# Kernel tuning notes

Measured on AMD Instinct MI355X. Metric: run time of the kernel, lower is better.

Reference implementation:

```python
import jax, jax.numpy as jnp
import numpy as np

EPS = 1e-6

def feature_map(x):
    # 'elu' feature map: elu(x) + 1 (positive feature map from Katharopoulos et al.)
    return jax.nn.elu(x) + 1.0

def setup_inputs() -> dict:
    key = jax.random.key(0)
    kq, kk, kv = jax.random.split(key, 3)
    B, L, H, D = 4, 2048, 16, 64
    q = jax.random.normal(kq, (B, L, H, D), dtype=jnp.float32)
    k = jax.random.normal(kk, (B, L, H, D), dtype=jnp.float32)
    v = jax.random.normal(kv, (B, L, H, D), dtype=jnp.float32)
    return {"q": q, "k": k, "v": v}

def reference(q, k, v):
    # q, k, v: [N, L, H, D]  (attention_mask=None -> causal linear attention)
    qf = feature_map(q)
    kf = feature_map(k)
    # normalizer: z[n,l,h] = sum_d qf[n,l,h,d] * cumsum_s<=l kf[n,s,h,d]
    z = jnp.einsum('nlhd,nlhd->nlh', qf, jnp.cumsum(kf, axis=1)) + EPS
    # causal_dot_product via scan over sequence with carry S[n,h,d,m]
    B, L, H, D = q.shape
    M = v.shape[-1]
    qs = jnp.moveaxis(qf, 1, 0)  # [L, N, H, D]
    ks = jnp.moveaxis(kf, 1, 0)
    vs = jnp.moveaxis(v, 1, 0)

    def step(S, qkv):
        ql, kl, vl = qkv                              # [N,H,D], [N,H,D], [N,H,M]
        S = S + jnp.einsum('nhd,nhm->nhdm', kl, vl)   # running sum of k v^T
        out = jnp.einsum('nhd,nhdm->nhm', ql, S)
        return S, out

    S0 = jnp.zeros((B, H, D, M), dtype=q.dtype)
    _, outs = jax.lax.scan(step, S0, (qs, ks, vs))    # outs: [L, N, H, M]
    v_ = jnp.moveaxis(outs, 0, 1)                     # [N, L, H, M]
    return v_ / z[..., None]
```

## Files before the change

### kernel.cpp

```cpp
#include <hip/hip_runtime.h>
#include <cstdint>

#define LL 2048
#define HH 16
#define DD 64
#define LSTR 1024
#define EPSF 1e-6f
#define PAD 72
#define SWZ(row, off) ((row)*PAD + ((off) ^ ((((row)>>3)&7)<<3)))

typedef __bf16 bf16x8 __attribute__((ext_vector_type(8)));
typedef float floatx4 __attribute__((ext_vector_type(4)));
typedef unsigned short ushortx8 __attribute__((ext_vector_type(8)));
typedef unsigned short ushortx4 __attribute__((ext_vector_type(4)));
typedef unsigned short ushortx2 __attribute__((ext_vector_type(2)));

static __device__ __forceinline__ float fmap(float x){ return x > 0.f ? x + 1.f : __expf(x); }
static __device__ __forceinline__ unsigned short f2bf(float f){
    return __builtin_bit_cast(unsigned short, static_cast<__bf16>(f));
}
static __device__ __forceinline__ float bf2f(unsigned short s){
    unsigned u = ((unsigned)s) << 16;
    return __builtin_bit_cast(float, u);
}
static __device__ __forceinline__ bf16x8 ldf(const unsigned short* p){
    return __builtin_bit_cast(bf16x8, *(const ushortx8*)p);
}

template<bool MAP>
static __device__ __forceinline__ void st_sd(unsigned short* base, int r, int c, float4 a, float4 b){
    if (MAP) {
        *(ushortx4*)(base + r*PAD + c)     = ushortx4{ f2bf(fmap(a.x)), f2bf(fmap(a.y)), f2bf(fmap(a.z)), f2bf(fmap(a.w)) };
        *(ushortx4*)(base + (r+1)*PAD + c) = ushortx4{ f2bf(fmap(b.x)), f2bf(fmap(b.y)), f2bf(fmap(b.z)), f2bf(fmap(b.w)) };
    } else {
        *(ushortx4*)(base + r*PAD + c)     = ushortx4{ f2bf(a.x), f2bf(a.y), f2bf(a.z), f2bf(a.w) };
        *(ushortx4*)(base + (r+1)*PAD + c) = ushortx4{ f2bf(b.x), f2bf(b.y), f2bf(b.z), f2bf(b.w) };
    }
}
template<bool MAP>
static __device__ __forceinline__ void st_tr(unsigned short* base, int r, int c, float4 a, float4 b){
    float aa[4] = {a.x, a.y, a.z, a.w}, bb[4] = {b.x, b.y, b.z, b.w};
#pragma unroll
    for (int e = 0; e < 4; ++e) {
        float x0 = MAP ? fmap(aa[e]) : aa[e];
        float x1 = MAP ? fmap(bb[e]) : bb[e];
        *(ushortx2*)(base + SWZ(c+e, r)) = ushortx2{ f2bf(x0), f2bf(x1) };
    }
}

__global__ __launch_bounds__(512) void kA(const float* __restrict__ kp, const float* __restrict__ vp,
                                          unsigned short* __restrict__ snap, float* __restrict__ ksnap)
{
    __shared__ __align__(16) unsigned short kft[2][DD*PAD];
    __shared__ __align__(16) unsigned short vtt[2][DD*PAD];
    const int blk = blockIdx.x;
    const int bh = blk >> 3, oct = blk & 7, b = bh >> 4, h = bh & 15;
    const int t = threadIdx.x;
    const int w = t >> 6, lane = t & 63, quad = lane >> 4, lr = lane & 15;
    const int m0 = 16*(w & 3), dth = (w >> 2) << 1;
    const int l0s = (t >> 4) * 2, col4 = (t & 15) << 2;

    floatx4 acc[2];
    acc[0] = floatx4{0.f,0.f,0.f,0.f};
    acc[1] = floatx4{0.f,0.f,0.f,0.f};
    float ksa = 0.f;

    const int64_t gb0 = ((int64_t)(b*LL + oct*256)*HH + h)*DD;
    {
        const float* gk = kp + gb0 + (int64_t)l0s*LSTR + col4;
        const float* gv = vp + gb0 + (int64_t)l0s*LSTR + col4;
        float4 ka = *(const float4*)gk, kb = *(const float4*)(gk + LSTR);
        float4 va = *(const float4*)gv, vb = *(const float4*)(gv + LSTR);
        st_tr<true >(kft[0], l0s, col4, ka, kb);
        st_tr<false>(vtt[0], l0s, col4, va, vb);
    }
    __syncthreads();

#pragma unroll 1
    for (int sc = 0; sc < 4; ++sc) {
        const int p = sc & 1;
        float4 ka, kb, va, vb;
        if (sc < 3) {
            const int64_t gb = gb0 + (int64_t)(sc+1)*DD*LSTR;
            const float* gk = kp + gb + (int64_t)l0s*LSTR + col4;
            const float* gv = vp + gb + (int64_t)l0s*LSTR + col4;
            ka = *(const float4*)gk; kb = *(const float4*)(gk + LSTR);
            va = *(const float4*)gv; vb = *(const float4*)(gv + LSTR);
        }
#pragma unroll
        for (int kk = 0; kk < 2; ++kk) {
            bf16x8 a = ldf(vtt[p] + SWZ(m0+lr, kk*32 + quad*8));
#pragma unroll
            for (int dtl = 0; dtl < 2; ++dtl) {
                bf16x8 bbf = ldf(kft[p] + SWZ((dth+dtl)*16+lr, kk*32 + quad*8));
                acc[dtl] = __builtin_amdgcn_mfma_f32_16x16x32_bf16(a, bbf, acc[dtl], 0, 0, 0);
            }
        }
        {
            unsigned short* so = snap + ((int64_t)blk*4 + sc)*4096;
#pragma unroll
            for (int dtl = 0; dtl < 2; ++dtl)
#pragma unroll
                for (int r = 0; r < 4; ++r)
                    so[(m0 + quad*4 + r)*DD + (dth+dtl)*16 + lr] = f2bf(acc[dtl][r]);
        }
        if (t < DD) {
#pragma unroll
            for (int jj = 0; jj < 8; ++jj) {
                ushortx8 u = *(const ushortx8*)(kft[p] + SWZ(t, jj*8));
#pragma unroll
                for (int e = 0; e < 8; ++e) ksa += bf2f(u[e]);
            }
            ksnap[((int64_t)blk*4 + sc)*DD + t] = ksa;
        }
        if (sc < 3) {
            st_tr<true >(kft[p^1], l0s, col4, ka, kb);
            st_tr<false>(vtt[p^1], l0s, col4, va, vb);
        }
        __syncthreads();
    }
}

__global__ __launch_bounds__(256, 4) void kC(const float* __restrict__ qp, const float* __restrict__ kp,
                                             const float* __restrict__ vp,
                                             const unsigned short* __restrict__ snap,
                                             const float* __restrict__ ksnap,
                                             float* __restrict__ outp)
{
    __shared__ __align__(16) unsigned short kfx[DD*PAD];
    __shared__ __align__(16) unsigned short vtt[DD*PAD];
    __shared__ __align__(16) unsigned short sld[DD*PAD];
    const int bid = blockIdx.x;
    const int bh = bid >> 5, c = bid & 31, b = bh >> 4, h = bh & 15;
    const int o = c >> 2, j = c & 3;
    const int t = threadIdx.x;
    const int w = t >> 6, lane = t & 63, quad = lane >> 4, lr = lane & 15;
    const int l0 = 16*w;
    const int64_t gbase = ((int64_t)(b*LL + c*DD)*HH + h)*DD;
    const int64_t so8 = (int64_t)bh*8;

    float qv[16];
    {
        const float* gq = qp + gbase + (int64_t)(l0+lr)*LSTR;
        float4 a0 = *(const float4*)(gq + quad*8);
        float4 a1 = *(const float4*)(gq + quad*8 + 4);
        float4 a2 = *(const float4*)(gq + 32 + quad*8);
        float4 a3 = *(const float4*)(gq + 32 + quad*8 + 4);
        qv[0]=fmap(a0.x); qv[1]=fmap(a0.y); qv[2]=fmap(a0.z); qv[3]=fmap(a0.w);
        qv[4]=fmap(a1.x); qv[5]=fmap(a1.y); qv[6]=fmap(a1.z); qv[7]=fmap(a1.w);
        qv[8]=fmap(a2.x); qv[9]=fmap(a2.y); qv[10]=fmap(a2.z); qv[11]=fmap(a2.w);
        qv[12]=fmap(a3.x); qv[13]=fmap(a3.y); qv[14]=fmap(a3.z); qv[15]=fmap(a3.w);
    }

    {
        const int sm = t >> 2, sd0 = (t & 3) << 4;
        float sa[16];
#pragma unroll
        for (int e = 0; e < 16; ++e) sa[e] = 0.f;
#pragma unroll
        for (int op = 0; op < 7; ++op)
            if (op < o) {
                const unsigned short* sp = snap + ((so8 + op)*4 + 3)*4096 + sm*DD + sd0;
                ushortx8 u0 = *(const ushortx8*)sp, u1 = *(const ushortx8*)(sp + 8);
#pragma unroll
                for (int e = 0; e < 8; ++e) { sa[e] += bf2f(u0[e]); sa[8+e] += bf2f(u1[e]); }
            }
        if (j > 0) {
            const unsigned short* sp = snap + ((so8 + o)*4 + (j-1))*4096 + sm*DD + sd0;
            ushortx8 u0 = *(const ushortx8*)sp, u1 = *(const ushortx8*)(sp + 8);
#pragma unroll
            for (int e = 0; e < 8; ++e) { sa[e] += bf2f(u0[e]); sa[8+e] += bf2f(u1[e]); }
        }
        ushortx8 w0, w1;
#pragma unroll
        for (int e = 0; e < 8; ++e) { w0[e] = f2bf(sa[e]); w1[e] = f2bf(sa[8+e]); }
        *(ushortx8*)(sld + sm*PAD + sd0)     = w0;
        *(ushortx8*)(sld + sm*PAD + sd0 + 8) = w1;
    }

    float zfull = 0.f;
    {
        float kp16[16];
#pragma unroll
        for (int e = 0; e < 16; ++e) kp16[e] = 0.f;
#pragma unroll
        for (int op = 0; op < 7; ++op)
            if (op < o) {
                const float* kb = ksnap + ((so8 + op)*4 + 3)*DD;
                float4 x0 = *(const float4*)(kb + quad*8);
                float4 x1 = *(const float4*)(kb + quad*8 + 4);
                float4 x2 = *(const float4*)(kb + 32 + quad*8);
                float4 x3 = *(const float4*)(kb + 32 + quad*8 + 4);
                kp16[0]+=x0.x; kp16[1]+=x0.y; kp16[2]+=x0.z; kp16[3]+=x0.w;
                kp16[4]+=x1.x; kp16[5]+=x1.y; kp16[6]+=x1.z; kp16[7]+=x1.w;
                kp16[8]+=x2.x; kp16[9]+=x2.y; kp16[10]+=x2.z; kp16[11]+=x2.w;
                kp16[12]+=x3.x; kp16[13]+=x3.y; kp16[14]+=x3.z; kp16[15]+=x3.w;
            }
        if (j > 0) {
            const float* kb = ksnap + ((so8 + o)*4 + (j-1))*DD;
            float4 x0 = *(const float4*)(kb + quad*8);
            float4 x1 = *(const float4*)(kb + quad*8 + 4);
            float4 x2 = *(const float4*)(kb + 32 + quad*8);
            float4 x3 = *(const float4*)(kb + 32 + quad*8 + 4);
            kp16[0]+=x0.x; kp16[1]+=x0.y; kp16[2]+=x0.z; kp16[3]+=x0.w;
            kp16[4]+=x1.x; kp16[5]+=x1.y; kp16[6]+=x1.z; kp16[7]+=x1.w;
            kp16[8]+=x2.x; kp16[9]+=x2.y; kp16[10]+=x2.z; kp16[11]+=x2.w;
            kp16[12]+=x3.x; kp16[13]+=x3.y; kp16[14]+=x3.z; kp16[15]+=x3.w;
        }
#pragma unroll
        for (int e = 0; e < 16; ++e) zfull += qv[e] * kp16[e];
        zfull += __shfl_xor(zfull, 16, 64);
        zfull += __shfl_xor(zfull, 32, 64);
    }

    bf16x8 aq0, aq1;
#pragma unroll
    for (int e = 0; e < 8; ++e) { aq0[e] = (__bf16)qv[e]; aq1[e] = (__bf16)qv[8+e]; }

#pragma unroll
    for (int i = 0; i < 2; ++i) {
        int flat = t + 256*i;
        int l0s = (flat >> 4) * 2, col = (flat & 15) << 2;
        const float* gk = kp + gbase + (int64_t)l0s*LSTR + col;
        const float* gv = vp + gbase + (int64_t)l0s*LSTR + col;
        float4 ka = *(const float4*)(gk), kb = *(const float4*)(gk + LSTR);
        float4 va = *(const float4*)(gv), vb = *(const float4*)(gv + LSTR);
        st_sd<true >(kfx, l0s, col, ka, kb);
        st_tr<false>(vtt, l0s, col, va, vb);
    }
    __syncthreads();

    floatx4 sc4[4];
#pragma unroll
    for (int tt = 0; tt < 4; ++tt) sc4[tt] = floatx4{0.f,0.f,0.f,0.f};
#pragma unroll
    for (int kk = 0; kk < 2; ++kk) {
        bf16x8 aqk = kk ? aq1 : aq0;
#pragma unroll
        for (int tt = 0; tt < 4; ++tt) {
            bf16x8 bb = ldf(kfx + (tt*16+lr)*PAD + kk*32 + quad*8);
            sc4[tt] = __builtin_amdgcn_mfma_f32_16x16x32_bf16(aqk, bb, sc4[tt], 0, 0, 0);
        }
    }
    __syncthreads();

    float zp[4] = {0.f,0.f,0.f,0.f};
#pragma unroll
    for (int tt = 0; tt < 4; ++tt)
#pragma unroll
        for (int r = 0; r < 4; ++r) {
            int row = l0 + quad*4 + r;
            int col = tt*16 + lr;
            float val = (col <= row) ? sc4[tt][r] : 0.f;
            zp[r] += val;
            kfx[row*PAD + col] = f2bf(val);
        }
#pragma unroll
    for (int m = 1; m < 16; m <<= 1)
#pragma unroll
        for (int r = 0; r < 4; ++r) zp[r] += __shfl_xor(zp[r], m, 64);
    float rz[4];
#pragma unroll
    for (int r = 0; r < 4; ++r) {
        zp[r] += __shfl(zfull, quad*20 + r, 64);
        rz[r] = 1.f / (zp[r] + EPSF);
    }

    floatx4 oa[4];
#pragma unroll
    for (int mt = 0; mt < 4; ++mt) oa[mt] = floatx4{0.f,0.f,0.f,0.f};
#pragma unroll
    for (int kk = 0; kk < 2; ++kk) {
        bf16x8 a2 = ldf(kfx + (l0+lr)*PAD + kk*32 + quad*8);
#pragma unroll
        for (int mt = 0; mt < 4; ++mt) {
            bf16x8 bv = ldf(vtt + SWZ(mt*16+lr, kk*32 + quad*8));
            oa[mt] = __builtin_amdgcn_mfma_f32_16x16x32_bf16(a2, bv, oa[mt], 0, 0, 0);
        }
    }
#pragma unroll
    for (int kk = 0; kk < 2; ++kk) {
        bf16x8 aqk = kk ? aq1 : aq0;
#pragma unroll
        for (int mt = 0; mt < 4; ++mt) {
            bf16x8 bs = ldf(sld + (mt*16+lr)*PAD + kk*32 + quad*8);
            oa[mt] = __builtin_amdgcn_mfma_f32_16x16x32_bf16(aqk, bs, oa[mt], 0, 0, 0);
        }
    }
#pragma unroll
    for (int r = 0; r < 4; ++r) {
        int row = l0 + quad*4 + r;
#pragma unroll
        for (int mt = 0; mt < 4; ++mt)
            outp[gbase + (int64_t)row*LSTR + mt*16 + lr] = oa[mt][r] * rz[r];
    }
}

extern "C" void kernel_launch(void* const* d_in, const int* in_sizes, int n_in,
                              void* d_out, int out_size, void* d_ws, size_t ws_size,
                              hipStream_t stream) {
    const float* q = (const float*)d_in[0];
    const float* k = (const float*)d_in[1];
    const float* v = (const float*)d_in[2];
    float* out = (float*)d_out;
    char* ws = (char*)d_ws;
    unsigned short* snap = (unsigned short*)ws;
    float* ksnap = (float*)(ws + (size_t)512*4*4096*2);
    kA<<<512,  512, 0, stream>>>(k, v, snap, ksnap);
    kC<<<2048, 256, 0, stream>>>(q, k, v, snap, ksnap, out);
}
```

Measured before the change: 157.5 us.

## Merge four chunk blocks into one looping block with double-buffered prefetch

```diff
diff --git a/kernel.cpp b/kernel.cpp
--- a/kernel.cpp
+++ b/kernel.cpp
@@ -53,8 +53,9 @@
 {
     __shared__ __align__(16) unsigned short kft[2][DD*PAD];
     __shared__ __align__(16) unsigned short vtt[2][DD*PAD];
-    const int blk = blockIdx.x;
-    const int bh = blk >> 3, oct = blk & 7, b = bh >> 4, h = bh & 15;
+    const int orig = blockIdx.x;
+    const int oct = orig >> 6, bh = orig & 63, b = bh >> 4, h = bh & 15;
+    const int64_t sblk = (int64_t)bh*8 + oct;
     const int t = threadIdx.x;
     const int w = t >> 6, lane = t & 63, quad = lane >> 4, lr = lane & 15;
     const int m0 = 16*(w & 3), dth = (w >> 2) << 1;
@@ -97,7 +98,7 @@
             }
         }
         {
-            unsigned short* so = snap + ((int64_t)blk*4 + sc)*4096;
+            unsigned short* so = snap + (sblk*4 + sc)*4096;
 #pragma unroll
             for (int dtl = 0; dtl < 2; ++dtl)
 #pragma unroll
@@ -111,7 +112,7 @@
 #pragma unroll
                 for (int e = 0; e < 8; ++e) ksa += bf2f(u[e]);
             }
-            ksnap[((int64_t)blk*4 + sc)*DD + t] = ksa;
+            ksnap[(sblk*4 + sc)*DD + t] = ksa;
         }
         if (sc < 3) {
             st_tr<true >(kft[p^1], l0s, col4, ka, kb);
@@ -121,178 +122,178 @@
     }
 }
 
-__global__ __launch_bounds__(256, 4) void kC(const float* __restrict__ qp, const float* __restrict__ kp,
+__global__ __launch_bounds__(512, 2) void kD(const float* __restrict__ qp, const float* __restrict__ kp,
                                              const float* __restrict__ vp,
                                              const unsigned short* __restrict__ snap,
                                              const float* __restrict__ ksnap,
                                              float* __restrict__ outp)
 {
-    __shared__ __align__(16) unsigned short kfx[DD*PAD];
-    __shared__ __align__(16) unsigned short vtt[DD*PAD];
+    __shared__ __align__(16) unsigned short qls[2][DD*PAD];
+    __shared__ __align__(16) unsigned short kfx[2][DD*PAD];
+    __shared__ __align__(16) unsigned short vtt[2][DD*PAD];
+    __shared__ __align__(16) unsigned short sct[DD*PAD];
     __shared__ __align__(16) unsigned short sld[DD*PAD];
-    const int bid = blockIdx.x;
-    const int bh = bid >> 5, c = bid & 31, b = bh >> 4, h = bh & 15;
-    const int o = c >> 2, j = c & 3;
+    __shared__ float zp2[2][DD];
+    __shared__ float kzb[DD];
+    __shared__ float kzs[2][DD];
+
+    const int orig = blockIdx.x;
+    const int o = orig >> 6, bh = orig & 63, b = bh >> 4, h = bh & 15;
     const int t = threadIdx.x;
     const int w = t >> 6, lane = t & 63, quad = lane >> 4, lr = lane & 15;
-    const int l0 = 16*w;
-    const int64_t gbase = ((int64_t)(b*LL + c*DD)*HH + h)*DD;
-    const int64_t so8 = (int64_t)bh*8;
-
-    float qv[16];
+    const int wi = w >> 1, wj = w & 1;
+    const int l0 = 16*wi;
+    const int l0s = (t >> 4) * 2, col4 = (t & 15) << 2;
+    const int sm = t >> 3, sd0 = (t & 7) << 3;
+    const int64_t bhb = ((int64_t)b*LL*HH + h)*DD;
+    const int64_t sb8 = (int64_t)bh*8;
+
+    float sbase[8];
+#pragma unroll
+    for (int e = 0; e < 8; ++e) sbase[e] = 0.f;
+#pragma unroll
+    for (int op = 0; op < 7; ++op)
+        if (op < o) {
+            ushortx8 u = *(const ushortx8*)(snap + ((sb8+op)*4 + 3)*4096 + sm*DD + sd0);
+#pragma unroll
+            for (int e = 0; e < 8; ++e) sbase[e] += bf2f(u[e]);
+        }
     {
-        const float* gq = qp + gbase + (int64_t)(l0+lr)*LSTR;
-        float4 a0 = *(const float4*)(gq + quad*8);
-        float4 a1 = *(const float4*)(gq + quad*8 + 4);
-        float4 a2 = *(const float4*)(gq + 32 + quad*8);
-        float4 a3 = *(const float4*)(gq + 32 + quad*8 + 4);
-        qv[0]=fmap(a0.x); qv[1]=fmap(a0.y); qv[2]=fmap(a0.z); qv[3]=fmap(a0.w);
-        qv[4]=fmap(a1.x); qv[5]=fmap(a1.y); qv[6]=fmap(a1.z); qv[7]=fmap(a1.w);
-        qv[8]=fmap(a2.x); qv[9]=fmap(a2.y); qv[10]=fmap(a2.z); qv[11]=fmap(a2.w);
-        qv[12]=fmap(a3.x); qv[13]=fmap(a3.y); qv[14]=fmap(a3.z); qv[15]=fmap(a3.w);
-    }
-
-    {
-        const int sm = t >> 2, sd0 = (t & 3) << 4;
-        float sa[16];
-#pragma unroll
-        for (int e = 0; e < 16; ++e) sa[e] = 0.f;
+        ushortx8 w0;
+#pragma unroll
+        for (int e = 0; e < 8; ++e) w0[e] = f2bf(sbase[e]);
+        *(ushortx8*)(sld + sm*PAD + sd0) = w0;
+    }
+    if (t < 16) {
+        float a0=0.f, a1=0.f, a2=0.f, a3=0.f;
 #pragma unroll
         for (int op = 0; op < 7; ++op)
             if (op < o) {
-                const unsigned short* sp = snap + ((so8 + op)*4 + 3)*4096 + sm*DD + sd0;
-                ushortx8 u0 = *(const ushortx8*)sp, u1 = *(const ushortx8*)(sp + 8);
-#pragma unroll
-                for (int e = 0; e < 8; ++e) { sa[e] += bf2f(u0[e]); sa[8+e] += bf2f(u1[e]); }
-            }
+                float4 x = *(const float4*)(ksnap + ((sb8+op)*4 + 3)*DD + t*4);
+                a0 += x.x; a1 += x.y; a2 += x.z; a3 += x.w;
+            }
+        *(float4*)(kzb + t*4) = float4{a0,a1,a2,a3};
+    }
+    {
+        const int64_t gb = bhb + (int64_t)(o*4)*DD*LSTR;
+        const float* gq = qp + gb + (int64_t)l0s*LSTR + col4;
+        const float* gk = kp + gb + (int64_t)l0s*LSTR + col4;
+        const float* gv = vp + gb + (int64_t)l0s*LSTR + col4;
+        float4 q0 = *(const float4*)gq, q1 = *(const float4*)(gq + LSTR);
+        float4 k0 = *(const float4*)gk, k1 = *(const float4*)(gk + LSTR);
+        float4 v0 = *(const float4*)gv, v1 = *(const float4*)(gv + LSTR);
+        st_sd<true >(qls[0], l0s, col4, q0, q1);
+        st_sd<true >(kfx[0], l0s, col4, k0, k1);
+        st_tr<false>(vtt[0], l0s, col4, v0, v1);
+    }
+    __syncthreads();
+
+    ushortx8 usn = ushortx8{0,0,0,0,0,0,0,0};
+    float4 cq0, cq1, ck0, ck1, cv0, cv1;
+
+#pragma unroll 1
+    for (int j = 0; j < 4; ++j) {
+        const int p = j & 1;
+        const int64_t gb = bhb + (int64_t)(o*4 + j)*DD*LSTR;
         if (j > 0) {
-            const unsigned short* sp = snap + ((so8 + o)*4 + (j-1))*4096 + sm*DD + sd0;
-            ushortx8 u0 = *(const ushortx8*)sp, u1 = *(const ushortx8*)(sp + 8);
-#pragma unroll
-            for (int e = 0; e < 8; ++e) { sa[e] += bf2f(u0[e]); sa[8+e] += bf2f(u1[e]); }
-        }
-        ushortx8 w0, w1;
-#pragma unroll
-        for (int e = 0; e < 8; ++e) { w0[e] = f2bf(sa[e]); w1[e] = f2bf(sa[8+e]); }
-        *(ushortx8*)(sld + sm*PAD + sd0)     = w0;
-        *(ushortx8*)(sld + sm*PAD + sd0 + 8) = w1;
-    }
-
-    float zfull = 0.f;
-    {
-        float kp16[16];
-#pragma unroll
-        for (int e = 0; e < 16; ++e) kp16[e] = 0.f;
-#pragma unroll
-        for (int op = 0; op < 7; ++op)
-            if (op < o) {
-                const float* kb = ksnap + ((so8 + op)*4 + 3)*DD;
-                float4 x0 = *(const float4*)(kb + quad*8);
-                float4 x1 = *(const float4*)(kb + quad*8 + 4);
-                float4 x2 = *(const float4*)(kb + 32 + quad*8);
-                float4 x3 = *(const float4*)(kb + 32 + quad*8 + 4);
-                kp16[0]+=x0.x; kp16[1]+=x0.y; kp16[2]+=x0.z; kp16[3]+=x0.w;
-                kp16[4]+=x1.x; kp16[5]+=x1.y; kp16[6]+=x1.z; kp16[7]+=x1.w;
-                kp16[8]+=x2.x; kp16[9]+=x2.y; kp16[10]+=x2.z; kp16[11]+=x2.w;
-                kp16[12]+=x3.x; kp16[13]+=x3.y; kp16[14]+=x3.z; kp16[15]+=x3.w;
-            }
-        if (j > 0) {
-            const float* kb = ksnap + ((so8 + o)*4 + (j-1))*DD;
-            float4 x0 = *(const float4*)(kb + quad*8);
-            float4 x1 = *(const float4*)(kb + quad*8 + 4);
-            float4 x2 = *(const float4*)(kb + 32 + quad*8);
-            float4 x3 = *(const float4*)(kb + 32 + quad*8 + 4);
-            kp16[0]+=x0.x; kp16[1]+=x0.y; kp16[2]+=x0.z; kp16[3]+=x0.w;
-            kp16[4]+=x1.x; kp16[5]+=x1.y; kp16[6]+=x1.z; kp16[7]+=x1.w;
-            kp16[8]+=x2.x; kp16[9]+=x2.y; kp16[10]+=x2.z; kp16[11]+=x2.w;
-            kp16[12]+=x3.x; kp16[13]+=x3.y; kp16[14]+=x3.z; kp16[15]+=x3.w;
-        }
-#pragma unroll
-        for (int e = 0; e < 16; ++e) zfull += qv[e] * kp16[e];
-        zfull += __shfl_xor(zfull, 16, 64);
-        zfull += __shfl_xor(zfull, 32, 64);
-    }
-
-    bf16x8 aq0, aq1;
-#pragma unroll
-    for (int e = 0; e < 8; ++e) { aq0[e] = (__bf16)qv[e]; aq1[e] = (__bf16)qv[8+e]; }
-
-#pragma unroll
-    for (int i = 0; i < 2; ++i) {
-        int flat = t + 256*i;
-        int l0s = (flat >> 4) * 2, col = (flat & 15) << 2;
-        const float* gk = kp + gbase + (int64_t)l0s*LSTR + col;
-        const float* gv = vp + gbase + (int64_t)l0s*LSTR + col;
-        float4 ka = *(const float4*)(gk), kb = *(const float4*)(gk + LSTR);
-        float4 va = *(const float4*)(gv), vb = *(const float4*)(gv + LSTR);
-        st_sd<true >(kfx, l0s, col, ka, kb);
-        st_tr<false>(vtt, l0s, col, va, vb);
-    }
-    __syncthreads();
-
-    floatx4 sc4[4];
-#pragma unroll
-    for (int tt = 0; tt < 4; ++tt) sc4[tt] = floatx4{0.f,0.f,0.f,0.f};
-#pragma unroll
-    for (int kk = 0; kk < 2; ++kk) {
-        bf16x8 aqk = kk ? aq1 : aq0;
-#pragma unroll
-        for (int tt = 0; tt < 4; ++tt) {
-            bf16x8 bb = ldf(kfx + (tt*16+lr)*PAD + kk*32 + quad*8);
-            sc4[tt] = __builtin_amdgcn_mfma_f32_16x16x32_bf16(aqk, bb, sc4[tt], 0, 0, 0);
-        }
-    }
-    __syncthreads();
-
-    float zp[4] = {0.f,0.f,0.f,0.f};
-#pragma unroll
-    for (int tt = 0; tt < 4; ++tt)
+            ushortx8 w0;
+#pragma unroll
+            for (int e = 0; e < 8; ++e) w0[e] = f2bf(sbase[e] + bf2f(usn[e]));
+            *(ushortx8*)(sld + sm*PAD + sd0) = w0;
+        }
+        bf16x8 aq0 = ldf(qls[p] + (l0+lr)*PAD + quad*8);
+        bf16x8 aq1 = ldf(qls[p] + (l0+lr)*PAD + 32 + quad*8);
+        float zfull = 0.f;
+        {
+            const float* kc = (j == 0) ? kzb : kzs[j & 1];
+#pragma unroll
+            for (int e = 0; e < 8; ++e) zfull += (float)aq0[e] * kc[quad*8 + e];
+#pragma unroll
+            for (int e = 0; e < 8; ++e) zfull += (float)aq1[e] * kc[32 + quad*8 + e];
+            zfull += __shfl_xor(zfull, 16, 64);
+            zfull += __shfl_xor(zfull, 32, 64);
+        }
+        if (j < 3) {
+            const int64_t gn = bhb + (int64_t)(o*4 + j + 1)*DD*LSTR;
+            const float* gq = qp + gn + (int64_t)l0s*LSTR + col4;
+            const float* gk = kp + gn + (int64_t)l0s*LSTR + col4;
+            const float* gv = vp + gn + (int64_t)l0s*LSTR + col4;
+            cq0 = *(const float4*)gq; cq1 = *(const float4*)(gq + LSTR);
+            ck0 = *(const float4*)gk; ck1 = *(const float4*)(gk + LSTR);
+            cv0 = *(const float4*)gv; cv1 = *(const float4*)(gv + LSTR);
+            usn = *(const ushortx8*)(snap + ((sb8+o)*4 + j)*4096 + sm*DD + sd0);
+            if (t < 16) {
+                float4 x = *(const float4*)(ksnap + ((sb8+o)*4 + j)*DD + t*4);
+                float4 zb = *(const float4*)(kzb + t*4);
+                *(float4*)(kzs[(j+1)&1] + t*4) = float4{zb.x+x.x, zb.y+x.y, zb.z+x.z, zb.w+x.w};
+            }
+        }
+        floatx4 s0 = floatx4{0.f,0.f,0.f,0.f}, s1 = floatx4{0.f,0.f,0.f,0.f};
+#pragma unroll
+        for (int kk = 0; kk < 2; ++kk) {
+            bf16x8 aqk = kk ? aq1 : aq0;
+            bf16x8 b0 = ldf(kfx[p] + ((2*wj+0)*16+lr)*PAD + kk*32 + quad*8);
+            bf16x8 b1 = ldf(kfx[p] + ((2*wj+1)*16+lr)*PAD + kk*32 + quad*8);
+            s0 = __builtin_amdgcn_mfma_f32_16x16x32_bf16(aqk, b0, s0, 0, 0, 0);
+            s1 = __builtin_amdgcn_mfma_f32_16x16x32_bf16(aqk, b1, s1, 0, 0, 0);
+        }
+        float zpv[4] = {0.f,0.f,0.f,0.f};
+#pragma unroll
+        for (int tt = 0; tt < 2; ++tt) {
+            int colb = (2*wj+tt)*16 + lr;
+            floatx4 sv = tt ? s1 : s0;
+#pragma unroll
+            for (int r = 0; r < 4; ++r) {
+                int row = l0 + quad*4 + r;
+                float val = (colb <= row) ? sv[r] : 0.f;
+                zpv[r] += val;
+                sct[row*PAD + colb] = f2bf(val);
+            }
+        }
+#pragma unroll
+        for (int m = 1; m < 16; m <<= 1)
+#pragma unroll
+            for (int r = 0; r < 4; ++r) zpv[r] += __shfl_xor(zpv[r], m, 64);
+        float zadd[4];
+#pragma unroll
+        for (int r = 0; r < 4; ++r) zadd[r] = __shfl(zfull, quad*20 + r, 64);
+        if (lr == 0) {
+#pragma unroll
+            for (int r = 0; r < 4; ++r)
+                zp2[wj][l0 + quad*4 + r] = zpv[r] + (wj == 0 ? zadd[r] : 0.f);
+        }
+        __syncthreads();
+
+        floatx4 oa0 = floatx4{0.f,0.f,0.f,0.f}, oa1 = floatx4{0.f,0.f,0.f,0.f};
+#pragma unroll
+        for (int kk = 0; kk < 2; ++kk) {
+            bf16x8 a2  = ldf(sct + (l0+lr)*PAD + kk*32 + quad*8);
+            bf16x8 bv0 = ldf(vtt[p] + SWZ((2*wj+0)*16+lr, kk*32 + quad*8));
+            bf16x8 bv1 = ldf(vtt[p] + SWZ((2*wj+1)*16+lr, kk*32 + quad*8));
+            oa0 = __builtin_amdgcn_mfma_f32_16x16x32_bf16(a2, bv0, oa0, 0, 0, 0);
+            oa1 = __builtin_amdgcn_mfma_f32_16x16x32_bf16(a2, bv1, oa1, 0, 0, 0);
+        }
+#pragma unroll
+        for (int kk = 0; kk < 2; ++kk) {
+            bf16x8 aqk = kk ? aq1 : aq0;
+            bf16x8 bs0 = ldf(sld + ((2*wj+0)*16+lr)*PAD + kk*32 + quad*8);
+            bf16x8 bs1 = ldf(sld + ((2*wj+1)*16+lr)*PAD + kk*32 + quad*8);
+            oa0 = __builtin_amdgcn_mfma_f32_16x16x32_bf16(aqk, bs0, oa0, 0, 0, 0);
+            oa1 = __builtin_amdgcn_mfma_f32_16x16x32_bf16(aqk, bs1, oa1, 0, 0, 0);
+        }
 #pragma unroll
         for (int r = 0; r < 4; ++r) {
             int row = l0 + quad*4 + r;
-            int col = tt*16 + lr;
-            float val = (col <= row) ? sc4[tt][r] : 0.f;
-            zp[r] += val;
-            kfx[row*PAD + col] = f2bf(val);
-        }
-#pragma unroll
-    for (int m = 1; m < 16; m <<= 1)
-#pragma unroll
-        for (int r = 0; r < 4; ++r) zp[r] += __shfl_xor(zp[r], m, 64);
-    float rz[4];
-#pragma unroll
-    for (int r = 0; r < 4; ++r) {
-        zp[r] += __shfl(zfull, quad*20 + r, 64);
-        rz[r] = 1.f / (zp[r] + EPSF);
-    }
-
-    floatx4 oa[4];
-#pragma unroll
-    for (int mt = 0; mt < 4; ++mt) oa[mt] = floatx4{0.f,0.f,0.f,0.f};
-#pragma unroll
-    for (int kk = 0; kk < 2; ++kk) {
-        bf16x8 a2 = ldf(kfx + (l0+lr)*PAD + kk*32 + quad*8);
-#pragma unroll
-        for (int mt = 0; mt < 4; ++mt) {
-            bf16x8 bv = ldf(vtt + SWZ(mt*16+lr, kk*32 + quad*8));
-            oa[mt] = __builtin_amdgcn_mfma_f32_16x16x32_bf16(a2, bv, oa[mt], 0, 0, 0);
-        }
-    }
-#pragma unroll
-    for (int kk = 0; kk < 2; ++kk) {
-        bf16x8 aqk = kk ? aq1 : aq0;
-#pragma unroll
-        for (int mt = 0; mt < 4; ++mt) {
-            bf16x8 bs = ldf(sld + (mt*16+lr)*PAD + kk*32 + quad*8);
-            oa[mt] = __builtin_amdgcn_mfma_f32_16x16x32_bf16(aqk, bs, oa[mt], 0, 0, 0);
-        }
-    }
-#pragma unroll
-    for (int r = 0; r < 4; ++r) {
-        int row = l0 + quad*4 + r;
-#pragma unroll
-        for (int mt = 0; mt < 4; ++mt)
-            outp[gbase + (int64_t)row*LSTR + mt*16 + lr] = oa[mt][r] * rz[r];
+            float rz = 1.f / (zp2[0][row] + zp2[1][row] + EPSF);
+            outp[gb + (int64_t)row*LSTR + (2*wj+0)*16 + lr] = oa0[r] * rz;
+            outp[gb + (int64_t)row*LSTR + (2*wj+1)*16 + lr] = oa1[r] * rz;
+        }
+        if (j < 3) {
+            st_sd<true >(qls[p^1], l0s, col4, cq0, cq1);
+            st_sd<true >(kfx[p^1], l0s, col4, ck0, ck1);
+            st_tr<false>(vtt[p^1], l0s, col4, cv0, cv1);
+        }
+        __syncthreads();
     }
 }
 
@@ -306,6 +307,6 @@
     char* ws = (char*)d_ws;
     unsigned short* snap = (unsigned short*)ws;
     float* ksnap = (float*)(ws + (size_t)512*4*4096*2);
-    kA<<<512,  512, 0, stream>>>(k, v, snap, ksnap);
-    kC<<<2048, 256, 0, stream>>>(q, k, v, snap, ksnap, out);
-}
+    kA<<<512, 512, 0, stream>>>(k, v, snap, ksnap);
+    kD<<<512, 512, 0, stream>>>(q, k, v, snap, ksnap, out);
+}
```

Result: no change. 155.4 us (-1.4%).
